# Performance work log

Hardware: AMD Instinct MI355X
Metric: run time of the kernel (lower is better)

Reference implementation:

```python
import jax, jax.numpy as jnp
import numpy as np

B, L, D_PAIR, N_HEAD = 1, 320, 128, 4
EPS = 1e-5


def setup_inputs() -> dict:
    key = jax.random.key(0)
    ks = jax.random.split(key, 8)
    s = 0.05  # ~xavier scale for fan_in=128
    return {
        "pair": jax.random.normal(ks[0], (B, L, L, D_PAIR), jnp.float32),
        "norm_w": jnp.ones((D_PAIR,), jnp.float32),
        "norm_b": jnp.zeros((D_PAIR,), jnp.float32),
        "Wq": jax.random.normal(ks[1], (D_PAIR, D_PAIR), jnp.float32) * s,
        "Wk": jax.random.normal(ks[2], (D_PAIR, D_PAIR), jnp.float32) * s,
        "Wv": jax.random.normal(ks[3], (D_PAIR, D_PAIR), jnp.float32) * s,
        "Wg": jax.random.normal(ks[4], (D_PAIR, D_PAIR), jnp.float32) * s,
        "bg": jnp.zeros((D_PAIR,), jnp.float32),
        "Wo": jax.random.normal(ks[5], (D_PAIR, D_PAIR), jnp.float32) * s,
        "bo": jnp.zeros((D_PAIR,), jnp.float32),
        "Wb": jax.random.normal(ks[6], (N_HEAD, D_PAIR), jnp.float32) * s,
    }


def reference(pair, norm_w, norm_b, Wq, Wk, Wv, Wg, bg, Wo, bo, Wb):
    # Triangle attention, mode='start' (no permute). pair: (B, L, L, D)
    Bs, Ls, _, D = pair.shape
    H = Wb.shape[0]
    Dh = D // H
    scale = Dh ** -0.5

    # LayerNorm (fp32, matches torch eps=1e-5)
    mu = jnp.mean(pair, axis=-1, keepdims=True)
    var = jnp.var(pair, axis=-1, keepdims=True)
    x = (pair - mu) * jax.lax.rsqrt(var + EPS) * norm_w + norm_b

    def heads(y):
        # (B,L,L,D) -> (B,L,H,L,Dh): attention runs along the second L axis per row i
        return y.reshape(Bs, Ls, Ls, H, Dh).transpose(0, 1, 3, 2, 4)

    Q = heads(x @ Wq.T)
    K = heads(x @ Wk.T)
    V = heads(x @ Wv.T)
    g = heads(jax.nn.sigmoid(x @ Wg.T + bg))

    attn = jnp.einsum('blhid,blhjd->blhij', Q, K) * scale  # (B,L,H,L,L)
    # bias from RAW pair (pre-norm), projected to heads, broadcast over query index i
    bias = (pair @ Wb.T).transpose(0, 1, 3, 2)[:, :, :, None, :]  # (B,L,H,1,L)
    attn = jax.nn.softmax(attn + bias, axis=-1)

    out = jnp.einsum('blhij,blhjd->blhid', attn, V)  # (B,L,H,L,Dh)
    out = (g * out).transpose(0, 1, 3, 2, 4).reshape(Bs, Ls, Ls, D)
    return pair + out @ Wo.T + bo
```

## Files before the change

### kernel.cpp

```cpp
#include <hip/hip_runtime.h>

typedef unsigned short u16;
typedef unsigned int u32;
typedef __attribute__((ext_vector_type(8))) short bf16x8;
typedef __attribute__((ext_vector_type(4))) float f32x4;
typedef __attribute__((ext_vector_type(2))) unsigned int u32x2;

#define LOG2E 1.4426950408889634f

__device__ __forceinline__ u16 f2bf(float f) {
    u32 u = __float_as_uint(f);
    u += 0x7fffu + ((u >> 16) & 1u);
    return (u16)(u >> 16);
}
__device__ __forceinline__ u32 pk_bf_trunc(float hi, float lo) {
    return __builtin_amdgcn_perm(__float_as_uint(hi), __float_as_uint(lo), 0x07060302u);
}

__global__ void wconv_kernel(const float* __restrict__ Wq, const float* __restrict__ Wk,
                             const float* __restrict__ Wv, const float* __restrict__ Wg,
                             const float* __restrict__ Wo, const float* __restrict__ norm_w,
                             const float* __restrict__ norm_b, const float* __restrict__ bg,
                             u16* __restrict__ wbf, float* __restrict__ cvec) {
    int b = blockIdx.x;
    if (b < 64) {
        int idx = b * 256 + threadIdx.x;
        float w = norm_w[idx & 127];
        wbf[0 * 16384 + idx] = f2bf(Wq[idx] * w);
        wbf[1 * 16384 + idx] = f2bf(Wk[idx] * w);
        wbf[2 * 16384 + idx] = f2bf(Wv[idx] * w);
        wbf[3 * 16384 + idx] = f2bf(Wg[idx] * w);
        wbf[4 * 16384 + idx] = f2bf(Wo[idx]);
    } else {
        int m = b - 64;
        int n = threadIdx.x;
        if (n < 128) {
            const float* W = (m == 0) ? Wq : (m == 1) ? Wk : (m == 2) ? Wv : Wg;
            float c = 0.f;
#pragma unroll
            for (int k4 = 0; k4 < 32; ++k4) {
                f32x4 bb = *(const f32x4*)&norm_b[k4 * 4];
                f32x4 ww = *(const f32x4*)&W[n * 128 + k4 * 4];
                c += bb[0] * ww[0] + bb[1] * ww[1] + bb[2] * ww[2] + bb[3] * ww[3];
            }
            if (m == 3) c += bg[n];
            cvec[m * 128 + n] = c;
        }
    }
}

#define KS_OFF 9216
#define VTS_OFF 22016
#define PB_W 1152

__global__ __launch_bounds__(512, 4)
void attn_kernel(const float* __restrict__ pair,
                 const float* __restrict__ Wb,
                 const u16* __restrict__ wbf,
                 const float* __restrict__ cvec,
                 u16* __restrict__ Obf,
                 u16* __restrict__ Gg) {
    const int bid = blockIdx.x;
    const int xcd = bid & 7;
    const int s_i = bid >> 3;
    const int h = s_i & 3;
    const int l = ((s_i >> 2) << 3) | xcd;
    const int tid = threadIdx.x;
    const int wave = tid >> 6;
    const int lane = tid & 63;
    const int i_lo = lane & 15;
    const int q = lane >> 4;

    __shared__ __align__(16) u16 smem[32576];
    __shared__ __align__(16) float biasLds[320];

    const int row_g = tid >> 3;
    const int c8 = tid & 7;
    const int wrow = (wave & 3) * 16;
    const int nth_flip = wave >> 2;

    f32x4 wbv[4];
#pragma unroll
    for (int u = 0; u < 4; ++u)
        wbv[u] = *(const f32x4*)&Wb[h * 128 + c8 * 16 + u * 4];

    float cQ[2], cK[2], cV[2], cG[2];
#pragma unroll
    for (int half = 0; half < 2; ++half) {
        int n = h * 32 + half * 16 + i_lo;
        cQ[half] = cvec[0 * 128 + n];
        cK[half] = cvec[1 * 128 + n];
        cV[half] = cvec[2 * 128 + n];
        cG[half] = cvec[3 * 128 + n];
    }

    u32 qkeep[3][4];

    const float* prowb = pair + ((size_t)(l * 320 + row_g)) * 128 + c8 * 16;
    f32x4 pr[4];
#pragma unroll
    for (int u = 0; u < 4; ++u) pr[u] = *(const f32x4*)(prowb + u * 4);

#pragma unroll 1
    for (int t = 0; t < 5; ++t) {
        const int j0 = t * 64;

        float s = 0.f, s2 = 0.f, bd = 0.f;
#pragma unroll
        for (int u = 0; u < 4; ++u) {
            f32x4 p = pr[u];
            f32x4 wb4 = wbv[u];
            s += p[0] + p[1] + p[2] + p[3];
            s2 += p[0] * p[0] + p[1] * p[1] + p[2] * p[2] + p[3] * p[3];
            bd += p[0] * wb4[0] + p[1] * wb4[1] + p[2] * wb4[2] + p[3] * wb4[3];
        }
        s += __shfl_xor(s, 1);   s += __shfl_xor(s, 2);   s += __shfl_xor(s, 4);
        s2 += __shfl_xor(s2, 1); s2 += __shfl_xor(s2, 2); s2 += __shfl_xor(s2, 4);
        bd += __shfl_xor(bd, 1); bd += __shfl_xor(bd, 2); bd += __shfl_xor(bd, 4);
        float mu = s * 0.0078125f;
        float var = s2 * 0.0078125f - mu * mu;
        float rs = rsqrtf(var + 1e-5f);

        __syncthreads();
#pragma unroll
        for (int u = 0; u < 4; ++u) {
            f32x4 p = pr[u];
            ushort4 xv;
            xv.x = f2bf((p[0] - mu) * rs);
            xv.y = f2bf((p[1] - mu) * rs);
            xv.z = f2bf((p[2] - mu) * rs);
            xv.w = f2bf((p[3] - mu) * rs);
            *(ushort4*)&smem[row_g * 136 + c8 * 16 + u * 4] = xv;
        }
        if (c8 == 0) biasLds[j0 + row_g] = bd * LOG2E;
        __syncthreads();

        if (t < 4) {
            const float* prow = prowb + (size_t)(t + 1) * 64 * 128;
#pragma unroll
            for (int u = 0; u < 4; ++u) pr[u] = *(const f32x4*)(prow + u * 4);
        }

        const int nth = (t & 1) ^ nth_flip;
        f32x4 acc[4];
#pragma unroll
        for (int n2 = 0; n2 < 4; ++n2) acc[n2] = (f32x4){0.f, 0.f, 0.f, 0.f};
#pragma unroll
        for (int kc = 0; kc < 4; ++kc) {
            bf16x8 a = *(const bf16x8*)&smem[(wrow + i_lo) * 136 + kc * 32 + q * 8];
#pragma unroll
            for (int n2 = 0; n2 < 4; ++n2) {
                int nt = nth * 4 + n2;
                bf16x8 wf = *(const bf16x8*)&wbf[(nt >> 1) * 16384 +
                                                 (h * 32 + (nt & 1) * 16 + i_lo) * 128 + kc * 32 + q * 8];
                acc[n2] = __builtin_amdgcn_mfma_f32_16x16x32_bf16(a, wf, acc[n2], 0, 0, 0);
            }
        }
        const int jrow = j0 + wrow + q * 4;
        if (nth == 0) {
            const int ti = t >> 1;
#pragma unroll
            for (int dd = 0; dd < 2; ++dd)
#pragma unroll
                for (int rr = 0; rr < 2; ++rr)
                    qkeep[ti][dd * 2 + rr] =
                        (u32)f2bf(acc[dd][rr * 2] + cQ[dd]) |
                        ((u32)f2bf(acc[dd][rr * 2 + 1] + cQ[dd]) << 16);
#pragma unroll
            for (int n2 = 2; n2 < 4; ++n2)
#pragma unroll
                for (int r = 0; r < 4; ++r)
                    smem[KS_OFF + (jrow + r) * 40 + (n2 & 1) * 16 + i_lo] =
                        f2bf(acc[n2][r] + cK[n2 & 1]);
        } else {
#pragma unroll
            for (int n2 = 0; n2 < 2; ++n2)
#pragma unroll
                for (int r = 0; r < 4; ++r)
                    smem[VTS_OFF + (n2 * 16 + i_lo) * 330 + jrow + r] =
                        f2bf(acc[n2][r] + cV[n2]);
#pragma unroll
            for (int n2 = 2; n2 < 4; ++n2)
#pragma unroll
                for (int r = 0; r < 4; ++r) {
                    float z = acc[n2][r] + cG[n2 & 1];
                    float g = 1.0f / (1.0f + exp2f(-z * LOG2E));
                    Gg[((size_t)((l * 4 + h) * 320 + jrow + r)) * 32 + (n2 & 1) * 16 + i_lo] = f2bf(g);
                }
        }
    }
    __syncthreads();

    const float SC = 0.17677669529663687f * LOG2E;
    const f32x4 zero4 = {0.f, 0.f, 0.f, 0.f};
    u16* pb = smem + wave * PB_W;
    const int nstrip = (wave < 4) ? 3 : 2;
#pragma unroll 1
    for (int t2 = 0; t2 < nstrip; ++t2) {
        const int i0 = (wave + 8 * t2) * 16;

        const size_t gbase = ((size_t)((l * 4 + h) * 320 + i0 + i_lo)) * 32;
        u32x2 gv0 = *(const u32x2*)&Gg[gbase + 0 * 16 + q * 4];
        u32x2 gv1 = *(const u32x2*)&Gg[gbase + 1 * 16 + q * 4];

#pragma unroll
        for (int dd = 0; dd < 2; ++dd)
#pragma unroll
            for (int rr = 0; rr < 2; ++rr) {
                u32 v = qkeep[t2][dd * 2 + rr];
                pb[(q * 4 + rr * 2) * 40 + dd * 16 + i_lo] = (u16)v;
                pb[(q * 4 + rr * 2 + 1) * 40 + dd * 16 + i_lo] = (u16)(v >> 16);
            }
        bf16x8 qf = *(const bf16x8*)&pb[i_lo * 40 + q * 8];

        f32x4 oacc[2];
        oacc[0] = zero4; oacc[1] = zero4;
        float sum = 0.f;

        f32x4 sc4[4];
#pragma unroll
        for (int jt = 0; jt < 4; ++jt) {
            bf16x8 kf = *(const bf16x8*)&smem[KS_OFF + (jt * 16 + i_lo) * 40 + q * 8];
            sc4[jt] = __builtin_amdgcn_mfma_f32_16x16x32_bf16(kf, qf, zero4, 0, 0, 0);
        }
#pragma unroll 1
        for (int c = 0; c < 5; ++c) {
#pragma unroll
            for (int jt = 0; jt < 4; ++jt) {
                f32x4 b4 = *(const f32x4*)&biasLds[c * 64 + jt * 16 + q * 4];
#pragma unroll
                for (int r = 0; r < 4; ++r) {
                    float p = exp2f(sc4[jt][r] * SC + b4[r]);
                    sc4[jt][r] = p;
                    sum += p;
                }
            }
#pragma unroll
            for (int jt = 0; jt < 4; ++jt) {
                u32x2 pk;
                pk.x = pk_bf_trunc(sc4[jt][1], sc4[jt][0]);
                pk.y = pk_bf_trunc(sc4[jt][3], sc4[jt][2]);
                *(u32x2*)&pb[i_lo * 72 + jt * 16 + q * 4] = pk;
            }
            f32x4 sc4n[4];
            if (c < 4) {
#pragma unroll
                for (int jt = 0; jt < 4; ++jt) {
                    bf16x8 kf = *(const bf16x8*)&smem[KS_OFF + ((c + 1) * 64 + jt * 16 + i_lo) * 40 + q * 8];
                    sc4n[jt] = __builtin_amdgcn_mfma_f32_16x16x32_bf16(kf, qf, zero4, 0, 0, 0);
                }
            }
            __builtin_amdgcn_s_setprio(1);
#pragma unroll
            for (int kt2 = 0; kt2 < 2; ++kt2) {
                bf16x8 pf = *(const bf16x8*)&pb[i_lo * 72 + kt2 * 32 + q * 8];
#pragma unroll
                for (int mt = 0; mt < 2; ++mt) {
                    bf16x8 vf = *(const bf16x8*)&smem[VTS_OFF + (mt * 16 + i_lo) * 330 +
                                                      c * 64 + kt2 * 32 + q * 8];
                    oacc[mt] = __builtin_amdgcn_mfma_f32_16x16x32_bf16(vf, pf, oacc[mt], 0, 0, 0);
                }
            }
            __builtin_amdgcn_s_setprio(0);
            if (c < 4) {
#pragma unroll
                for (int jt = 0; jt < 4; ++jt) sc4[jt] = sc4n[jt];
            }
        }

        sum += __shfl_xor(sum, 16);
        sum += __shfl_xor(sum, 32);
        float rinv = 1.0f / sum;
#pragma unroll
        for (int mt = 0; mt < 2; ++mt) {
            u32x2 gv = mt ? gv1 : gv0;
            float g0 = __uint_as_float(gv.x << 16);
            float g1 = __uint_as_float(gv.x & 0xffff0000u);
            float g2 = __uint_as_float(gv.y << 16);
            float g3 = __uint_as_float(gv.y & 0xffff0000u);
            u32x2 pk;
            pk.x = pk_bf_trunc(oacc[mt][1] * rinv * g1, oacc[mt][0] * rinv * g0);
            pk.y = pk_bf_trunc(oacc[mt][3] * rinv * g3, oacc[mt][2] * rinv * g2);
            *(u32x2*)&Obf[((size_t)(l * 320 + i0 + i_lo)) * 128 + h * 32 + mt * 16 + q * 4] = pk;
        }
    }
}

__global__ __launch_bounds__(256, 4)
void outproj_kernel(const float* __restrict__ pair,
                    const float* __restrict__ bo,
                    const u16* __restrict__ Obf,
                    const u16* __restrict__ wbf,
                    float* __restrict__ out) {
    const int tid = threadIdx.x;
    const int wave = tid >> 6;
    const int lane = tid & 63;
    const int i_lo = lane & 15;
    const int q = lane >> 4;

    __shared__ __align__(16) u16 WoLds[128 * 128];

    const int row0 = blockIdx.x * 64 + wave * 16;

    bf16x8 of[4];
#pragma unroll
    for (int kc = 0; kc < 4; ++kc)
        of[kc] = *(const bf16x8*)&Obf[((size_t)(row0 + i_lo)) * 128 + kc * 32 + q * 8];

    const u16* Wo = wbf + 4 * 16384;
#pragma unroll
    for (int it = 0; it < 8; ++it) {
        int unit = it * 256 + tid;
        int n = unit >> 4, k8 = unit & 15;
        *(bf16x8*)&WoLds[n * 128 + ((k8 ^ (n & 15)) * 8)] = *(const bf16x8*)&Wo[unit * 8];
    }
    __syncthreads();

    f32x4 acc[8];
#pragma unroll
    for (int nt = 0; nt < 8; ++nt) acc[nt] = (f32x4){0.f, 0.f, 0.f, 0.f};
#pragma unroll
    for (int nt = 0; nt < 8; ++nt) {
#pragma unroll
        for (int kc = 0; kc < 4; ++kc) {
            bf16x8 wf = *(const bf16x8*)&WoLds[(nt * 16 + i_lo) * 128 + (((kc * 4 + q) ^ i_lo) * 8)];
            acc[nt] = __builtin_amdgcn_mfma_f32_16x16x32_bf16(wf, of[kc], acc[nt], 0, 0, 0);
        }
    }
#pragma unroll
    for (int nt = 0; nt < 8; ++nt) {
        size_t idx = ((size_t)(row0 + i_lo)) * 128 + nt * 16 + q * 4;
        f32x4 p4 = *(const f32x4*)&pair[idx];
        f32x4 b4 = *(const f32x4*)&bo[nt * 16 + q * 4];
        f32x4 o4;
        o4[0] = acc[nt][0] + p4[0] + b4[0];
        o4[1] = acc[nt][1] + p4[1] + b4[1];
        o4[2] = acc[nt][2] + p4[2] + b4[2];
        o4[3] = acc[nt][3] + p4[3] + b4[3];
        *(f32x4*)&out[idx] = o4;
    }
}

extern "C" void kernel_launch(void* const* d_in, const int* in_sizes, int n_in,
                              void* d_out, int out_size, void* d_ws, size_t ws_size,
                              hipStream_t stream) {
    const float* pair   = (const float*)d_in[0];
    const float* norm_w = (const float*)d_in[1];
    const float* norm_b = (const float*)d_in[2];
    const float* Wq     = (const float*)d_in[3];
    const float* Wk     = (const float*)d_in[4];
    const float* Wv     = (const float*)d_in[5];
    const float* Wg     = (const float*)d_in[6];
    const float* bg     = (const float*)d_in[7];
    const float* Wo     = (const float*)d_in[8];
    const float* bo     = (const float*)d_in[9];
    const float* Wb     = (const float*)d_in[10];

    u16* wbf    = (u16*)d_ws;
    float* cvec = (float*)(wbf + 5 * 16384);
    u16* Obf    = (u16*)(cvec + 512);
    u16* Gg     = Obf + (size_t)102400 * 128;
    float* out  = (float*)d_out;

    wconv_kernel<<<68, 256, 0, stream>>>(Wq, Wk, Wv, Wg, Wo, norm_w, norm_b, bg, wbf, cvec);
    attn_kernel<<<320 * 4, 512, 0, stream>>>(pair, Wb, wbf, cvec, Obf, Gg);
    outproj_kernel<<<1600, 256, 0, stream>>>(pair, bo, Obf, wbf, out);
}
```

Baseline: 281.8 us.

## Split LayerNorm into separate kernel and use register-permuted P with swizzled LDS

Moves LayerNorm and the pair-bias projection into a new ln_kernel that writes normalized bf16 rows and per-head bias to scratch in the output buffer. The attention kernel no longer recomputes LayerNorm four times per row (once per head) and loads X fragments straight from global memory. It also swizzles the K and V^T LDS layouts to avoid bank conflicts, and passes the softmax probabilities via ds_bpermute instead of an LDS round trip. The smaller LDS footprint allows raising launch bounds to 6 blocks. The cost is an extra kernel launch plus a bf16 X write and read through global memory, and it drops the software pipelining of the QK MFMA across chunks.

```diff
diff --git a/kernel.cpp b/kernel.cpp
--- a/kernel.cpp
+++ b/kernel.cpp
@@ -49,13 +49,70 @@
     }
 }
 
-#define KS_OFF 9216
-#define VTS_OFF 22016
-#define PB_W 1152
-
-__global__ __launch_bounds__(512, 4)
-void attn_kernel(const float* __restrict__ pair,
-                 const float* __restrict__ Wb,
+__global__ __launch_bounds__(512)
+void ln_kernel(const float* __restrict__ pair, const float* __restrict__ Wb,
+               u16* __restrict__ Xbf, float* __restrict__ biasT) {
+    const int bid = blockIdx.x;
+    const int xcd = bid & 7;
+    const int s = bid >> 3;
+    const int jc = s % 5;
+    const int l = (s / 5) * 8 + xcd;
+    const int j0 = jc * 64;
+    const int tid = threadIdx.x;
+    const int row_g = tid >> 3;
+    const int c8 = tid & 7;
+
+    const size_t row = (size_t)(l * 320 + j0 + row_g);
+    const float* prow = pair + row * 128 + c8 * 16;
+    f32x4 pr[4];
+#pragma unroll
+    for (int u = 0; u < 4; ++u) pr[u] = *(const f32x4*)(prow + u * 4);
+
+    float s1 = 0.f, s2 = 0.f;
+    float bd[4] = {0.f, 0.f, 0.f, 0.f};
+#pragma unroll
+    for (int u = 0; u < 4; ++u) {
+        f32x4 p = pr[u];
+        s1 += p[0] + p[1] + p[2] + p[3];
+        s2 += p[0] * p[0] + p[1] * p[1] + p[2] * p[2] + p[3] * p[3];
+#pragma unroll
+        for (int hh = 0; hh < 4; ++hh) {
+            f32x4 w4 = *(const f32x4*)&Wb[hh * 128 + c8 * 16 + u * 4];
+            bd[hh] += p[0] * w4[0] + p[1] * w4[1] + p[2] * w4[2] + p[3] * w4[3];
+        }
+    }
+    s1 += __shfl_xor(s1, 1); s1 += __shfl_xor(s1, 2); s1 += __shfl_xor(s1, 4);
+    s2 += __shfl_xor(s2, 1); s2 += __shfl_xor(s2, 2); s2 += __shfl_xor(s2, 4);
+#pragma unroll
+    for (int hh = 0; hh < 4; ++hh) {
+        bd[hh] += __shfl_xor(bd[hh], 1);
+        bd[hh] += __shfl_xor(bd[hh], 2);
+        bd[hh] += __shfl_xor(bd[hh], 4);
+    }
+    float mu = s1 * 0.0078125f;
+    float var = s2 * 0.0078125f - mu * mu;
+    float rs = rsqrtf(var + 1e-5f);
+
+#pragma unroll
+    for (int u = 0; u < 4; ++u) {
+        f32x4 p = pr[u];
+        ushort4 xv;
+        xv.x = f2bf((p[0] - mu) * rs);
+        xv.y = f2bf((p[1] - mu) * rs);
+        xv.z = f2bf((p[2] - mu) * rs);
+        xv.w = f2bf((p[3] - mu) * rs);
+        *(ushort4*)&Xbf[row * 128 + c8 * 16 + u * 4] = xv;
+    }
+    if (c8 < 4) biasT[((size_t)l * 4 + c8) * 320 + j0 + row_g] = bd[c8];
+}
+
+#define PB_OFF 0
+#define KS_OFF 5120
+#define VTS_OFF 15360
+
+__global__ __launch_bounds__(512, 6)
+void attn_kernel(const u16* __restrict__ Xbf,
+                 const float* __restrict__ biasT,
                  const u16* __restrict__ wbf,
                  const float* __restrict__ cvec,
                  u16* __restrict__ Obf,
@@ -71,18 +128,13 @@
     const int i_lo = lane & 15;
     const int q = lane >> 4;
 
-    __shared__ __align__(16) u16 smem[32576];
+    __shared__ __align__(16) u16 smem[25600];
     __shared__ __align__(16) float biasLds[320];
 
-    const int row_g = tid >> 3;
-    const int c8 = tid & 7;
     const int wrow = (wave & 3) * 16;
     const int nth_flip = wave >> 2;
 
-    f32x4 wbv[4];
-#pragma unroll
-    for (int u = 0; u < 4; ++u)
-        wbv[u] = *(const f32x4*)&Wb[h * 128 + c8 * 16 + u * 4];
+    if (tid < 320) biasLds[tid] = biasT[((size_t)l * 4 + h) * 320 + tid] * LOG2E;
 
     float cQ[2], cK[2], cV[2], cG[2];
 #pragma unroll
@@ -96,50 +148,14 @@
 
     u32 qkeep[3][4];
 
-    const float* prowb = pair + ((size_t)(l * 320 + row_g)) * 128 + c8 * 16;
-    f32x4 pr[4];
-#pragma unroll
-    for (int u = 0; u < 4; ++u) pr[u] = *(const f32x4*)(prowb + u * 4);
-
 #pragma unroll 1
     for (int t = 0; t < 5; ++t) {
         const int j0 = t * 64;
-
-        float s = 0.f, s2 = 0.f, bd = 0.f;
-#pragma unroll
-        for (int u = 0; u < 4; ++u) {
-            f32x4 p = pr[u];
-            f32x4 wb4 = wbv[u];
-            s += p[0] + p[1] + p[2] + p[3];
-            s2 += p[0] * p[0] + p[1] * p[1] + p[2] * p[2] + p[3] * p[3];
-            bd += p[0] * wb4[0] + p[1] * wb4[1] + p[2] * wb4[2] + p[3] * wb4[3];
-        }
-        s += __shfl_xor(s, 1);   s += __shfl_xor(s, 2);   s += __shfl_xor(s, 4);
-        s2 += __shfl_xor(s2, 1); s2 += __shfl_xor(s2, 2); s2 += __shfl_xor(s2, 4);
-        bd += __shfl_xor(bd, 1); bd += __shfl_xor(bd, 2); bd += __shfl_xor(bd, 4);
-        float mu = s * 0.0078125f;
-        float var = s2 * 0.0078125f - mu * mu;
-        float rs = rsqrtf(var + 1e-5f);
-
-        __syncthreads();
-#pragma unroll
-        for (int u = 0; u < 4; ++u) {
-            f32x4 p = pr[u];
-            ushort4 xv;
-            xv.x = f2bf((p[0] - mu) * rs);
-            xv.y = f2bf((p[1] - mu) * rs);
-            xv.z = f2bf((p[2] - mu) * rs);
-            xv.w = f2bf((p[3] - mu) * rs);
-            *(ushort4*)&smem[row_g * 136 + c8 * 16 + u * 4] = xv;
-        }
-        if (c8 == 0) biasLds[j0 + row_g] = bd * LOG2E;
-        __syncthreads();
-
-        if (t < 4) {
-            const float* prow = prowb + (size_t)(t + 1) * 64 * 128;
-#pragma unroll
-            for (int u = 0; u < 4; ++u) pr[u] = *(const f32x4*)(prow + u * 4);
-        }
+        bf16x8 xf[4];
+#pragma unroll
+        for (int kc = 0; kc < 4; ++kc)
+            xf[kc] = *(const bf16x8*)&Xbf[((size_t)(l * 320 + j0 + wrow + i_lo)) * 128 +
+                                          kc * 32 + q * 8];
 
         const int nth = (t & 1) ^ nth_flip;
         f32x4 acc[4];
@@ -147,13 +163,12 @@
         for (int n2 = 0; n2 < 4; ++n2) acc[n2] = (f32x4){0.f, 0.f, 0.f, 0.f};
 #pragma unroll
         for (int kc = 0; kc < 4; ++kc) {
-            bf16x8 a = *(const bf16x8*)&smem[(wrow + i_lo) * 136 + kc * 32 + q * 8];
 #pragma unroll
             for (int n2 = 0; n2 < 4; ++n2) {
                 int nt = nth * 4 + n2;
                 bf16x8 wf = *(const bf16x8*)&wbf[(nt >> 1) * 16384 +
                                                  (h * 32 + (nt & 1) * 16 + i_lo) * 128 + kc * 32 + q * 8];
-                acc[n2] = __builtin_amdgcn_mfma_f32_16x16x32_bf16(a, wf, acc[n2], 0, 0, 0);
+                acc[n2] = __builtin_amdgcn_mfma_f32_16x16x32_bf16(xf[kc], wf, acc[n2], 0, 0, 0);
             }
         }
         const int jrow = j0 + wrow + q * 4;
@@ -167,18 +182,26 @@
                         (u32)f2bf(acc[dd][rr * 2] + cQ[dd]) |
                         ((u32)f2bf(acc[dd][rr * 2 + 1] + cQ[dd]) << 16);
 #pragma unroll
-            for (int n2 = 2; n2 < 4; ++n2)
+            for (int n2 = 2; n2 < 4; ++n2) {
+                const int uK = (2 * (n2 & 1) + (i_lo >> 3)) ^ q;
 #pragma unroll
                 for (int r = 0; r < 4; ++r)
-                    smem[KS_OFF + (jrow + r) * 40 + (n2 & 1) * 16 + i_lo] =
+                    smem[KS_OFF + (jrow + r) * 32 + uK * 8 + (i_lo & 7)] =
                         f2bf(acc[n2][r] + cK[n2 & 1]);
+            }
         } else {
 #pragma unroll
-            for (int n2 = 0; n2 < 2; ++n2)
-#pragma unroll
-                for (int r = 0; r < 4; ++r)
-                    smem[VTS_OFF + (n2 * 16 + i_lo) * 330 + jrow + r] =
+            for (int n2 = 0; n2 < 2; ++n2) {
+                const int dv = n2 * 16 + i_lo;
+#pragma unroll
+                for (int r = 0; r < 4; ++r) {
+                    const int j = jrow + r;
+                    const int uu = j >> 3;
+                    const int uh = (uu & ~7) | ((uu & 7) ^ (i_lo & 7));
+                    smem[VTS_OFF + dv * 320 + uh * 8 + (j & 7)] =
                         f2bf(acc[n2][r] + cV[n2]);
+                }
+            }
 #pragma unroll
             for (int n2 = 2; n2 < 4; ++n2)
 #pragma unroll
@@ -193,8 +216,12 @@
 
     const float SC = 0.17677669529663687f * LOG2E;
     const f32x4 zero4 = {0.f, 0.f, 0.f, 0.f};
-    u16* pb = smem + wave * PB_W;
+    u16* pb = smem + PB_OFF + wave * 640;
     const int nstrip = (wave < 4) ? 3 : 2;
+    const int kswz = (q ^ (i_lo >> 2)) * 8;
+    const int la4 = (((lane & 16) << 1) | i_lo) * 4;
+    const int lb4 = la4 + 64;
+    const bool hi = (lane >= 32);
 #pragma unroll 1
     for (int t2 = 0; t2 < nstrip; ++t2) {
         const int i0 = (wave + 8 * t2) * 16;
@@ -216,15 +243,14 @@
         f32x4 oacc[2];
         oacc[0] = zero4; oacc[1] = zero4;
         float sum = 0.f;
-
-        f32x4 sc4[4];
-#pragma unroll
-        for (int jt = 0; jt < 4; ++jt) {
-            bf16x8 kf = *(const bf16x8*)&smem[KS_OFF + (jt * 16 + i_lo) * 40 + q * 8];
-            sc4[jt] = __builtin_amdgcn_mfma_f32_16x16x32_bf16(kf, qf, zero4, 0, 0, 0);
-        }
 #pragma unroll 1
         for (int c = 0; c < 5; ++c) {
+            f32x4 sc4[4];
+#pragma unroll
+            for (int jt = 0; jt < 4; ++jt) {
+                bf16x8 kf = *(const bf16x8*)&smem[KS_OFF + (c * 64 + jt * 16 + i_lo) * 32 + kswz];
+                sc4[jt] = __builtin_amdgcn_mfma_f32_16x16x32_bf16(kf, qf, zero4, 0, 0, 0);
+            }
 #pragma unroll
             for (int jt = 0; jt < 4; ++jt) {
                 f32x4 b4 = *(const f32x4*)&biasLds[c * 64 + jt * 16 + q * 4];
@@ -235,37 +261,38 @@
                     sum += p;
                 }
             }
+            u32 pkx[4], pky[4];
 #pragma unroll
             for (int jt = 0; jt < 4; ++jt) {
-                u32x2 pk;
-                pk.x = pk_bf_trunc(sc4[jt][1], sc4[jt][0]);
-                pk.y = pk_bf_trunc(sc4[jt][3], sc4[jt][2]);
-                *(u32x2*)&pb[i_lo * 72 + jt * 16 + q * 4] = pk;
-            }
-            f32x4 sc4n[4];
-            if (c < 4) {
-#pragma unroll
-                for (int jt = 0; jt < 4; ++jt) {
-                    bf16x8 kf = *(const bf16x8*)&smem[KS_OFF + ((c + 1) * 64 + jt * 16 + i_lo) * 40 + q * 8];
-                    sc4n[jt] = __builtin_amdgcn_mfma_f32_16x16x32_bf16(kf, qf, zero4, 0, 0, 0);
+                pkx[jt] = pk_bf_trunc(sc4[jt][1], sc4[jt][0]);
+                pky[jt] = pk_bf_trunc(sc4[jt][3], sc4[jt][2]);
+            }
+            __builtin_amdgcn_s_setprio(1);
+#pragma unroll
+            for (int kt2 = 0; kt2 < 2; ++kt2) {
+                const int jA = 2 * kt2, jB = jA + 1;
+                u32 a0 = (u32)__builtin_amdgcn_ds_bpermute(la4, (int)pkx[jA]);
+                u32 b0 = (u32)__builtin_amdgcn_ds_bpermute(la4, (int)pkx[jB]);
+                u32 a1 = (u32)__builtin_amdgcn_ds_bpermute(la4, (int)pky[jA]);
+                u32 b1 = (u32)__builtin_amdgcn_ds_bpermute(la4, (int)pky[jB]);
+                u32 a2 = (u32)__builtin_amdgcn_ds_bpermute(lb4, (int)pkx[jA]);
+                u32 b2 = (u32)__builtin_amdgcn_ds_bpermute(lb4, (int)pkx[jB]);
+                u32 a3 = (u32)__builtin_amdgcn_ds_bpermute(lb4, (int)pky[jA]);
+                u32 b3 = (u32)__builtin_amdgcn_ds_bpermute(lb4, (int)pky[jB]);
+                union { bf16x8 v; u32 u[4]; } pf;
+                pf.u[0] = hi ? b0 : a0;
+                pf.u[1] = hi ? b1 : a1;
+                pf.u[2] = hi ? b2 : a2;
+                pf.u[3] = hi ? b3 : a3;
+                const int vswz = ((4 * kt2 + q) ^ (i_lo & 7)) * 8;
+#pragma unroll
+                for (int mt = 0; mt < 2; ++mt) {
+                    bf16x8 vf = *(const bf16x8*)&smem[VTS_OFF + (mt * 16 + i_lo) * 320 +
+                                                      c * 64 + vswz];
+                    oacc[mt] = __builtin_amdgcn_mfma_f32_16x16x32_bf16(vf, pf.v, oacc[mt], 0, 0, 0);
                 }
             }
-            __builtin_amdgcn_s_setprio(1);
-#pragma unroll
-            for (int kt2 = 0; kt2 < 2; ++kt2) {
-                bf16x8 pf = *(const bf16x8*)&pb[i_lo * 72 + kt2 * 32 + q * 8];
-#pragma unroll
-                for (int mt = 0; mt < 2; ++mt) {
-                    bf16x8 vf = *(const bf16x8*)&smem[VTS_OFF + (mt * 16 + i_lo) * 330 +
-                                                      c * 64 + kt2 * 32 + q * 8];
-                    oacc[mt] = __builtin_amdgcn_mfma_f32_16x16x32_bf16(vf, pf, oacc[mt], 0, 0, 0);
-                }
-            }
             __builtin_amdgcn_s_setprio(0);
-            if (c < 4) {
-#pragma unroll
-                for (int jt = 0; jt < 4; ++jt) sc4[jt] = sc4n[jt];
-            }
         }
 
         sum += __shfl_xor(sum, 16);
@@ -362,7 +389,11 @@
     u16* Gg     = Obf + (size_t)102400 * 128;
     float* out  = (float*)d_out;
 
+    u16* Xbf     = (u16*)d_out;
+    float* biasT = (float*)((char*)d_out + 26214400);
+
     wconv_kernel<<<68, 256, 0, stream>>>(Wq, Wk, Wv, Wg, Wo, norm_w, norm_b, bg, wbf, cvec);
-    attn_kernel<<<320 * 4, 512, 0, stream>>>(pair, Wb, wbf, cvec, Obf, Gg);
+    ln_kernel<<<1600, 512, 0, stream>>>(pair, Wb, Xbf, biasT);
+    attn_kernel<<<320 * 4, 512, 0, stream>>>(Xbf, biasT, wbf, cvec, Obf, Gg);
     outproj_kernel<<<1600, 256, 0, stream>>>(pair, bo, Obf, wbf, out);
 }
```

New measurement: 312.3 us. 1.11x slower.

## Fuse output projection into attention kernel via per-head atomic accumulation

Applied to the files above, without the earlier changes.

Removes the separate out-projection kernel and the bf16 Obf intermediate. Each attention block multiplies its per-head gated output by the matching Wo column slice and atomically adds the partial result into the fp32 output. The output is first initialised to pair + bo inside the weight-conversion kernel. This saves the write and re-read of the intermediate and one launch, but adds four-way fp32 atomic contention per element, scattered 4-byte atomics, and makes the summation order nondeterministic.

```diff
diff --git a/kernel.cpp b/kernel.cpp
--- a/kernel.cpp
+++ b/kernel.cpp
@@ -21,7 +21,9 @@
                              const float* __restrict__ Wv, const float* __restrict__ Wg,
                              const float* __restrict__ Wo, const float* __restrict__ norm_w,
                              const float* __restrict__ norm_b, const float* __restrict__ bg,
-                             u16* __restrict__ wbf, float* __restrict__ cvec) {
+                             const float* __restrict__ pairIn, const float* __restrict__ bo,
+                             u16* __restrict__ wbf, float* __restrict__ cvec,
+                             float* __restrict__ outInit) {
     int b = blockIdx.x;
     if (b < 64) {
         int idx = b * 256 + threadIdx.x;
@@ -31,7 +33,7 @@
         wbf[2 * 16384 + idx] = f2bf(Wv[idx] * w);
         wbf[3 * 16384 + idx] = f2bf(Wg[idx] * w);
         wbf[4 * 16384 + idx] = f2bf(Wo[idx]);
-    } else {
+    } else if (b < 68) {
         int m = b - 64;
         int n = threadIdx.x;
         if (n < 128) {
@@ -46,6 +48,21 @@
             if (m == 3) c += bg[n];
             cvec[m * 128 + n] = c;
         }
+    } else {
+        const size_t base = (size_t)(b - 68) * 16384 + threadIdx.x * 4;
+        const int col = (threadIdx.x * 4) & 127;
+        f32x4 b4 = *(const f32x4*)&bo[col];
+#pragma unroll
+        for (int it = 0; it < 16; ++it) {
+            size_t idx = base + (size_t)it * 1024;
+            f32x4 p4 = *(const f32x4*)&pairIn[idx];
+            f32x4 o4;
+            o4[0] = p4[0] + b4[0];
+            o4[1] = p4[1] + b4[1];
+            o4[2] = p4[2] + b4[2];
+            o4[3] = p4[3] + b4[3];
+            *(f32x4*)&outInit[idx] = o4;
+        }
     }
 }
 
@@ -58,7 +75,7 @@
                  const float* __restrict__ Wb,
                  const u16* __restrict__ wbf,
                  const float* __restrict__ cvec,
-                 u16* __restrict__ Obf,
+                 float* __restrict__ out,
                  u16* __restrict__ Gg) {
     const int bid = blockIdx.x;
     const int xcd = bid & 7;
@@ -271,6 +288,7 @@
         sum += __shfl_xor(sum, 16);
         sum += __shfl_xor(sum, 32);
         float rinv = 1.0f / sum;
+
 #pragma unroll
         for (int mt = 0; mt < 2; ++mt) {
             u32x2 gv = mt ? gv1 : gv0;
@@ -281,63 +299,18 @@
             u32x2 pk;
             pk.x = pk_bf_trunc(oacc[mt][1] * rinv * g1, oacc[mt][0] * rinv * g0);
             pk.y = pk_bf_trunc(oacc[mt][3] * rinv * g3, oacc[mt][2] * rinv * g2);
-            *(u32x2*)&Obf[((size_t)(l * 320 + i0 + i_lo)) * 128 + h * 32 + mt * 16 + q * 4] = pk;
-        }
-    }
-}
-
-__global__ __launch_bounds__(256, 4)
-void outproj_kernel(const float* __restrict__ pair,
-                    const float* __restrict__ bo,
-                    const u16* __restrict__ Obf,
-                    const u16* __restrict__ wbf,
-                    float* __restrict__ out) {
-    const int tid = threadIdx.x;
-    const int wave = tid >> 6;
-    const int lane = tid & 63;
-    const int i_lo = lane & 15;
-    const int q = lane >> 4;
-
-    __shared__ __align__(16) u16 WoLds[128 * 128];
-
-    const int row0 = blockIdx.x * 64 + wave * 16;
-
-    bf16x8 of[4];
-#pragma unroll
-    for (int kc = 0; kc < 4; ++kc)
-        of[kc] = *(const bf16x8*)&Obf[((size_t)(row0 + i_lo)) * 128 + kc * 32 + q * 8];
-
-    const u16* Wo = wbf + 4 * 16384;
-#pragma unroll
-    for (int it = 0; it < 8; ++it) {
-        int unit = it * 256 + tid;
-        int n = unit >> 4, k8 = unit & 15;
-        *(bf16x8*)&WoLds[n * 128 + ((k8 ^ (n & 15)) * 8)] = *(const bf16x8*)&Wo[unit * 8];
-    }
-    __syncthreads();
-
-    f32x4 acc[8];
-#pragma unroll
-    for (int nt = 0; nt < 8; ++nt) acc[nt] = (f32x4){0.f, 0.f, 0.f, 0.f};
-#pragma unroll
-    for (int nt = 0; nt < 8; ++nt) {
-#pragma unroll
-        for (int kc = 0; kc < 4; ++kc) {
-            bf16x8 wf = *(const bf16x8*)&WoLds[(nt * 16 + i_lo) * 128 + (((kc * 4 + q) ^ i_lo) * 8)];
-            acc[nt] = __builtin_amdgcn_mfma_f32_16x16x32_bf16(wf, of[kc], acc[nt], 0, 0, 0);
-        }
-    }
-#pragma unroll
-    for (int nt = 0; nt < 8; ++nt) {
-        size_t idx = ((size_t)(row0 + i_lo)) * 128 + nt * 16 + q * 4;
-        f32x4 p4 = *(const f32x4*)&pair[idx];
-        f32x4 b4 = *(const f32x4*)&bo[nt * 16 + q * 4];
-        f32x4 o4;
-        o4[0] = acc[nt][0] + p4[0] + b4[0];
-        o4[1] = acc[nt][1] + p4[1] + b4[1];
-        o4[2] = acc[nt][2] + p4[2] + b4[2];
-        o4[3] = acc[nt][3] + p4[3] + b4[3];
-        *(f32x4*)&out[idx] = o4;
+            *(u32x2*)&pb[i_lo * 32 + mt * 16 + q * 4] = pk;
+        }
+        bf16x8 ogf = *(const bf16x8*)&pb[i_lo * 32 + q * 8];
+        float* outRow = out + ((size_t)(l * 320 + i0 + q * 4)) * 128 + i_lo;
+#pragma unroll
+        for (int ntile = 0; ntile < 8; ++ntile) {
+            bf16x8 wof = *(const bf16x8*)&wbf[4 * 16384 + (ntile * 16 + i_lo) * 128 + h * 32 + q * 8];
+            f32x4 pc = __builtin_amdgcn_mfma_f32_16x16x32_bf16(ogf, wof, zero4, 0, 0, 0);
+#pragma unroll
+            for (int r = 0; r < 4; ++r)
+                atomicAdd(&outRow[(size_t)r * 128 + ntile * 16], pc[r]);
+        }
     }
 }
 
@@ -358,11 +331,10 @@
 
     u16* wbf    = (u16*)d_ws;
     float* cvec = (float*)(wbf + 5 * 16384);
-    u16* Obf    = (u16*)(cvec + 512);
-    u16* Gg     = Obf + (size_t)102400 * 128;
+    u16* Gg     = (u16*)(cvec + 512);
     float* out  = (float*)d_out;
 
-    wconv_kernel<<<68, 256, 0, stream>>>(Wq, Wk, Wv, Wg, Wo, norm_w, norm_b, bg, wbf, cvec);
-    attn_kernel<<<320 * 4, 512, 0, stream>>>(pair, Wb, wbf, cvec, Obf, Gg);
-    outproj_kernel<<<1600, 256, 0, stream>>>(pair, bo, Obf, wbf, out);
-}
+    wconv_kernel<<<868, 256, 0, stream>>>(Wq, Wk, Wv, Wg, Wo, norm_w, norm_b, bg,
+                                          pair, bo, wbf, cvec, out);
+    attn_kernel<<<320 * 4, 512, 0, stream>>>(pair, Wb, wbf, cvec, out, Gg);
+}
```

Measured after the change: 375.1 us. 1.33x slower.
